# Kernel optimization log

Hardware: AMD Instinct MI355X
Metric: run time of the kernel (lower is better)

The kernel has to match this reference:

```python
import jax, jax.numpy as jnp
import numpy as np

L = 2
NB = (L + 1) ** 2      # 9 spherical-harmonic basis components
C = 256                # in_channels == out_channels
MID = C // 4           # 64, mid_channels in the FF
N = 4096               # nodes
K = 16                 # neighbors (neighbor_cg)


def _real_sh_l2(rel):
    # Real spherical harmonics up to l=2 of normalized edge directions. rel: [N,K,3] -> [N,K,9]
    r = jnp.sqrt(jnp.sum(rel * rel, axis=-1, keepdims=True))
    d = rel / (r + 1e-8)
    x, y, z = d[..., 0], d[..., 1], d[..., 2]
    c0 = 0.28209479177387814
    c1 = 0.4886025119029199
    c2 = 1.0925484305920792
    c2b = 0.31539156525252005
    c2c = 0.5462742152960396
    return jnp.stack([
        jnp.full_like(x, c0),
        c1 * y, c1 * z, c1 * x,
        c2 * x * y, c2 * y * z, c2b * (3.0 * z * z - 1.0), c2 * x * z, c2c * (x * x - y * y),
    ], axis=-1)


def setup_inputs() -> dict:
    key = jax.random.key(0)
    ks = jax.random.split(key, 8)
    return {
        "s_feats": jax.random.normal(ks[0], (N, NB, C), jnp.float32),
        "s_points": jax.random.normal(ks[1], (N, 3), jnp.float32),
        "cg": jax.random.normal(ks[2], (NB, NB, NB), jnp.float32) * 0.1,  # CG coefficient buffer
        "W_proj": jax.random.normal(ks[3], (C, C), jnp.float32) / np.sqrt(C),
        "ln_w": jnp.ones((L + 1, C), jnp.float32),
        "ln_b": jnp.zeros((C,), jnp.float32),
        "W_ff1": jax.random.normal(ks[4], (C, MID), jnp.float32) / np.sqrt(C),
        "W_gate": jax.random.normal(ks[5], (MID, MID * (L + 1)), jnp.float32) / np.sqrt(MID),
        "W_ff2": jax.random.normal(ks[6], (MID, C), jnp.float32) / np.sqrt(MID),
        "neighbor_indices": jax.random.randint(ks[7], (N, K), 0, N),
    }


def _forward(s_feats, s_points, cg, W_proj, ln_w, ln_b, W_ff1, W_gate, W_ff2, neighbor_indices):
    # --- CGConv: project, gather neighbors, SH of edge directions, CG tensor product, mean-aggregate ---
    h = jnp.einsum('nic,co->nio', s_feats, W_proj)               # [N,9,C]
    nbr = h[neighbor_indices]                                    # [N,K,9,C] irregular gather
    rel = s_points[neighbor_indices] - s_points[:, None, :]      # [N,K,3]
    sh = _real_sh_l2(rel)                                        # [N,K,9]
    x = jnp.einsum('nkic,nkj,ijo->noc', nbr, sh, cg) / K         # [N,9,C]
    # --- residual add of input (linear3 == Identity since in_channels == out_channels) ---
    x = x + s_feats
    shortcut = x
    # --- EquivariantLayerNormV2: per-degree RMS norm; mean-center + bias only on l=0 ---
    outs = []
    for l in range(L + 1):
        f = x[:, l * l:(l + 1) * (l + 1), :]                     # [N,2l+1,C]
        if l == 0:
            f = f - jnp.mean(f, axis=-1, keepdims=True)
        nrm = jnp.mean(f * f, axis=(1, 2), keepdims=True)
        f = f * jax.lax.rsqrt(nrm + 1e-5) * ln_w[l][None, None, :]
        if l == 0:
            f = f + ln_b[None, None, :]
        outs.append(f)
    y = jnp.concatenate(outs, axis=1)
    # --- FF: Linear -> Gate_3j -> Linear, residual ---
    z = jnp.einsum('nic,cm->nim', y, W_ff1)                      # [N,9,MID]
    after = z[:, 0, :] @ W_gate                                  # [N, MID*(L+1)]
    t0 = jax.nn.silu(after[:, :MID])
    mult = jax.nn.sigmoid(after[:, MID:])                        # [N, MID*L]
    gated = [t0[:, None, :]]
    for l in range(1, L + 1):
        gated.append(z[:, l * l:(l + 1) * (l + 1), :] * mult[:, None, (l - 1) * MID:l * MID])
    z = jnp.concatenate(gated, axis=1)                           # [N,9,MID]
    return jnp.einsum('nim,mc->nic', z, W_ff2) + shortcut


def reference(s_feats, s_points, cg, W_proj, ln_w, ln_b, W_ff1, W_gate, W_ff2, neighbor_indices):
    return _forward(s_feats, s_points, cg, W_proj, ln_w, ln_b, W_ff1, W_gate, W_ff2, neighbor_indices)
```

## Files before the change

kernel.cpp:

```cpp
#include <hip/hip_runtime.h>
#include <hip/hip_bf16.h>

#define N_PTS  4096
#define NB     9
#define C      256
#define MID    64
#define KNBR   16
#define NROWS  (N_PTS * NB)

typedef __attribute__((ext_vector_type(8))) short          short8;
typedef __attribute__((ext_vector_type(4))) float          f32x4;
typedef __attribute__((ext_vector_type(4))) unsigned short ush4;
typedef __attribute__((ext_vector_type(8))) unsigned short ush8;

static __device__ __forceinline__ unsigned short f2bf(float f) {
    union { __hip_bfloat16 h; unsigned short u; } cv;
    cv.h = __float2bfloat16(f);
    return cv.u;
}
static __device__ __forceinline__ float bf2f(unsigned short s) {
    union { unsigned u; float f; } v; v.u = ((unsigned)s) << 16;
    return v.f;
}
static __device__ __forceinline__ unsigned packbf(float a, float b) {
    return (unsigned)f2bf(a) | ((unsigned)f2bf(b) << 16);
}

__global__ __launch_bounds__(256) void k_prep(const float* __restrict__ Wp,
                                              const float* __restrict__ W1,
                                              const float* __restrict__ W2,
                                              unsigned short* __restrict__ Wpt,
                                              unsigned short* __restrict__ W1t,
                                              unsigned short* __restrict__ W2t) {
    __shared__ float T[32][33];
    const int b = blockIdx.x;
    const float* in; unsigned short* out; int K, N, kt, nt;
    if (b < 64)      { in = Wp; out = Wpt; K = 256; N = 256; kt = b >> 3;        nt = b & 7; }
    else if (b < 80) { in = W1; out = W1t; K = 256; N = 64;  kt = (b - 64) >> 1; nt = (b - 64) & 1; }
    else             { in = W2; out = W2t; K = 64;  N = 256; kt = (b - 80) >> 3; nt = (b - 80) & 7; }
    const int tx = threadIdx.x & 31;
    const int ty = threadIdx.x >> 5;
    const int k0 = kt * 32, n0 = nt * 32;
#pragma unroll
    for (int i = 0; i < 4; ++i)
        T[ty + i * 8][tx] = in[(size_t)(k0 + ty + i * 8) * N + n0 + tx];
    __syncthreads();
#pragma unroll
    for (int i = 0; i < 4; ++i)
        out[(size_t)(n0 + ty + i * 8) * K + k0 + tx] = f2bf(T[tx][ty + i * 8]);
}

#define LDK 40
__global__ __launch_bounds__(256) void k_proj(const float* __restrict__ A,
                                              const unsigned short* __restrict__ Wpt,
                                              unsigned short* __restrict__ H) {
    __shared__ unsigned short As[128 * LDK];
    __shared__ unsigned short Bs[128 * LDK];
    const int tid = threadIdx.x;
    const int r0  = blockIdx.x * 128;
    const int n0  = blockIdx.y * 128;
    const int wave = tid >> 6, lane = tid & 63;
    const int wm = wave >> 1, wn = wave & 1;
    const int lr = lane & 15, lg = lane >> 4;

    f32x4 acc[4][4];
#pragma unroll
    for (int a = 0; a < 4; ++a)
#pragma unroll
        for (int b = 0; b < 4; ++b) acc[a][b] = (f32x4){0.f, 0.f, 0.f, 0.f};

    for (int k0 = 0; k0 < C; k0 += 32) {
        __syncthreads();
#pragma unroll
        for (int rep = 0; rep < 4; ++rep) {
            const int e   = rep * 256 + tid;
            const int row = e >> 3;
            const int c4  = (e & 7) << 2;
            const float4 v = *reinterpret_cast<const float4*>(&A[(size_t)(r0 + row) * C + k0 + c4]);
            ush4 s = { f2bf(v.x), f2bf(v.y), f2bf(v.z), f2bf(v.w) };
            *reinterpret_cast<ush4*>(&As[row * LDK + c4]) = s;
        }
#pragma unroll
        for (int rep = 0; rep < 2; ++rep) {
            const int u   = rep * 256 + tid;
            const int row = u >> 2;
            const int seg = u & 3;
            *reinterpret_cast<ush8*>(&Bs[row * LDK + seg * 8]) =
                *reinterpret_cast<const ush8*>(&Wpt[(size_t)(n0 + row) * C + k0 + seg * 8]);
        }
        __syncthreads();

        short8 af[4], bfr[4];
#pragma unroll
        for (int mf = 0; mf < 4; ++mf)
            af[mf] = *reinterpret_cast<const short8*>(&As[(wm * 64 + mf * 16 + lr) * LDK + lg * 8]);
#pragma unroll
        for (int nf = 0; nf < 4; ++nf)
            bfr[nf] = *reinterpret_cast<const short8*>(&Bs[(wn * 64 + nf * 16 + lr) * LDK + lg * 8]);
#pragma unroll
        for (int mf = 0; mf < 4; ++mf)
#pragma unroll
            for (int nf = 0; nf < 4; ++nf)
                acc[mf][nf] = __builtin_amdgcn_mfma_f32_16x16x32_bf16(af[mf], bfr[nf], acc[mf][nf], 0, 0, 0);
    }
#pragma unroll
    for (int mf = 0; mf < 4; ++mf)
#pragma unroll
        for (int nf = 0; nf < 4; ++nf) {
            const int col = n0 + wn * 64 + nf * 16 + lr;
#pragma unroll
            for (int r = 0; r < 4; ++r) {
                const int row = r0 + wm * 64 + mf * 16 + lg * 4 + r;
                H[(size_t)row * C + col] = f2bf(acc[mf][nf][r]);
            }
        }
}

static __device__ __forceinline__ void load_chunk(const unsigned short* __restrict__ Hb,
                                                  const int* idx_s, int ki, int s,
                                                  ush8& q0, ush8& q1, ush8& q2, ush8& q3) {
    const int kk = ki / 9;
    const int ii = ki - kk * 9;
    const unsigned short* hrow = Hb + (size_t)(idx_s[kk] * NB + ii) * C + s * 32;
    q0 = *reinterpret_cast<const ush8*>(hrow + 0);
    q1 = *reinterpret_cast<const ush8*>(hrow + 8);
    q2 = *reinterpret_cast<const ush8*>(hrow + 16);
    q3 = *reinterpret_cast<const ush8*>(hrow + 24);
}
static __device__ __forceinline__ void stage_chunk(unsigned short* Bs, int r, int s, int nrows,
                                                   ush8 q0, ush8 q1, ush8 q2, ush8 q3) {
    if (r < nrows) {
        const unsigned short* qe;
        qe = reinterpret_cast<const unsigned short*>(&q0);
#pragma unroll
        for (int e = 0; e < 8; ++e) Bs[(s * 32 + e) * 40 + r] = qe[e];
        qe = reinterpret_cast<const unsigned short*>(&q1);
#pragma unroll
        for (int e = 0; e < 8; ++e) Bs[(s * 32 + 8 + e) * 40 + r] = qe[e];
        qe = reinterpret_cast<const unsigned short*>(&q2);
#pragma unroll
        for (int e = 0; e < 8; ++e) Bs[(s * 32 + 16 + e) * 40 + r] = qe[e];
        qe = reinterpret_cast<const unsigned short*>(&q3);
#pragma unroll
        for (int e = 0; e < 8; ++e) Bs[(s * 32 + 24 + e) * 40 + r] = qe[e];
    }
}

__global__ __launch_bounds__(256) void k_cg_ln(const unsigned short* __restrict__ Hb,
                                               const float* __restrict__ s_feats,
                                               const float* __restrict__ pts,
                                               const float* __restrict__ cg,
                                               const int*   __restrict__ nbr,
                                               unsigned short* __restrict__ Xb,
                                               float* __restrict__ scr) {
    __shared__ unsigned short Bs[256 * 40];
    __shared__ unsigned short wT[16 * 168];
    __shared__ float sh_s[KNBR][NB];
    __shared__ int   idx_s[KNBR];
    __shared__ float red_s[2][4];

    float* const cg_s = reinterpret_cast<float*>(Bs);

    const int tid  = threadIdx.x;
    const int n    = blockIdx.x;
    const int wv   = tid >> 6;
    const int lane = tid & 63;
    const int g16  = lane >> 4;
    const int l16  = lane & 15;

    {
        unsigned* w32 = reinterpret_cast<unsigned*>(wT);
        for (int e = tid; e < (16 * 168) / 2; e += 256) w32[e] = 0u;
    }
    for (int e = tid; e < 729; e += 256) cg_s[e] = cg[e];
    if (tid < KNBR) {
        const int idx = nbr[n * KNBR + tid];
        idx_s[tid] = idx;
        const float px = pts[idx * 3 + 0] - pts[n * 3 + 0];
        const float py = pts[idx * 3 + 1] - pts[n * 3 + 1];
        const float pz = pts[idx * 3 + 2] - pts[n * 3 + 2];
        const float r  = sqrtf(px * px + py * py + pz * pz);
        const float iv = 1.f / (r + 1e-8f);
        const float dx = px * iv, dy = py * iv, dz = pz * iv;
        const float c1 = 0.4886025119029199f;
        const float c2 = 1.0925484305920792f;
        sh_s[tid][0] = 0.28209479177387814f;
        sh_s[tid][1] = c1 * dy;
        sh_s[tid][2] = c1 * dz;
        sh_s[tid][3] = c1 * dx;
        sh_s[tid][4] = c2 * dx * dy;
        sh_s[tid][5] = c2 * dy * dz;
        sh_s[tid][6] = 0.31539156525252005f * (3.f * dz * dz - 1.f);
        sh_s[tid][7] = c2 * dx * dz;
        sh_s[tid][8] = 0.5462742152960396f * (dx * dx - dy * dy);
    }
    __syncthreads();

    const int r = tid & 31;
    const int s = tid >> 5;

    ush8 qa0, qa1, qa2, qa3, qb0, qb1, qb2, qb3;
    load_chunk(Hb, idx_s, 0 * 32 + r, s, qa0, qa1, qa2, qa3);
    load_chunk(Hb, idx_s, 1 * 32 + r, s, qb0, qb1, qb2, qb3);

    for (int t = tid; t < 144 * 9; t += 256) {
        const int ki = t / 9;
        const int o  = t - ki * 9;
        const int kk = ki / 9;
        const int ii = ki - kk * 9;
        float sv = 0.f;
#pragma unroll
        for (int j = 0; j < 9; ++j) sv = fmaf(sh_s[kk][j], cg_s[ii * 81 + j * 9 + o], sv);
        wT[o * 168 + ki] = f2bf(sv);
    }

    f32x4 acc[4];
#pragma unroll
    for (int i = 0; i < 4; ++i) acc[i] = (f32x4){0.f, 0.f, 0.f, 0.f};

#define MFMA_STEP(cc)                                                                   \
    do {                                                                                \
        const short8 af = *reinterpret_cast<const short8*>(&wT[l16 * 168 + (cc) * 32 + g16 * 8]); \
        short8 bfr[4];                                                                  \
        _Pragma("unroll")                                                               \
        for (int ti = 0; ti < 4; ++ti)                                                  \
            bfr[ti] = *reinterpret_cast<const short8*>(&Bs[(wv * 64 + ti * 16 + l16) * 40 + g16 * 8]); \
        _Pragma("unroll")                                                               \
        for (int ti = 0; ti < 4; ++ti)                                                  \
            acc[ti] = __builtin_amdgcn_mfma_f32_16x16x32_bf16(af, bfr[ti], acc[ti], 0, 0, 0); \
    } while (0)

    __syncthreads();
    stage_chunk(Bs, r, s, 32, qa0, qa1, qa2, qa3);
    load_chunk(Hb, idx_s, 2 * 32 + r, s, qa0, qa1, qa2, qa3);
    __syncthreads();
    MFMA_STEP(0);
    __syncthreads();
    stage_chunk(Bs, r, s, 32, qb0, qb1, qb2, qb3);
    load_chunk(Hb, idx_s, 3 * 32 + r, s, qb0, qb1, qb2, qb3);
    __syncthreads();
    MFMA_STEP(1);
    __syncthreads();
    stage_chunk(Bs, r, s, 32, qa0, qa1, qa2, qa3);
    if (r < 16) load_chunk(Hb, idx_s, 4 * 32 + r, s, qa0, qa1, qa2, qa3);
    __syncthreads();
    MFMA_STEP(2);
    __syncthreads();
    stage_chunk(Bs, r, s, 32, qb0, qb1, qb2, qb3);
    __syncthreads();
    MFMA_STEP(3);
    __syncthreads();
    stage_chunk(Bs, r, s, 16, qa0, qa1, qa2, qa3);
    __syncthreads();
    MFMA_STEP(4);
#undef MFMA_STEP

    __syncthreads();
    float* const Dld = reinterpret_cast<float*>(Bs);
#pragma unroll
    for (int ti = 0; ti < 4; ++ti) {
        const int cgl = (wv * 4 + ti) * 16 + l16;
#pragma unroll
        for (int rr = 0; rr < 4; ++rr) {
            const int o = g16 * 4 + rr;
            if (o < 9) Dld[o * 264 + cgl] = acc[ti][rr] * (1.f / (float)KNBR);
        }
    }
    __syncthreads();

    if (tid < 128) {
        const int c = tid * 2;
        const float* sf = s_feats + (size_t)n * (NB * C) + c;
        float2 xv[9];
#pragma unroll
        for (int i = 0; i < 9; ++i) {
            const float2 sv = *reinterpret_cast<const float2*>(&sf[(size_t)i * C]);
            xv[i].x = Dld[i * 264 + c]     + sv.x;
            xv[i].y = Dld[i * 264 + c + 1] + sv.y;
        }
        unsigned* xo = reinterpret_cast<unsigned*>(Xb + (size_t)n * (NB * C));
#pragma unroll
        for (int i = 0; i < 9; ++i) xo[i * 128 + tid] = packbf(xv[i].x, xv[i].y);

        float s0 = xv[0].x + xv[0].y;
        float s1 = xv[0].x * xv[0].x + xv[0].y * xv[0].y;
        float s2 = 0.f, s3 = 0.f;
#pragma unroll
        for (int o = 1; o < 4; ++o) s2 += xv[o].x * xv[o].x + xv[o].y * xv[o].y;
#pragma unroll
        for (int o = 4; o < 9; ++o) s3 += xv[o].x * xv[o].x + xv[o].y * xv[o].y;
#pragma unroll
        for (int off = 32; off >= 1; off >>= 1) {
            s0 += __shfl_xor(s0, off);
            s1 += __shfl_xor(s1, off);
            s2 += __shfl_xor(s2, off);
            s3 += __shfl_xor(s3, off);
        }
        if (lane == 0) {
            red_s[wv][0] = s0; red_s[wv][1] = s1;
            red_s[wv][2] = s2; red_s[wv][3] = s3;
        }
    }
    __syncthreads();
    if (tid == 0) {
        float* sp = scr + (size_t)n * 4;
        sp[0] = red_s[0][0] + red_s[1][0];
        sp[1] = red_s[0][1] + red_s[1][1];
        sp[2] = red_s[0][2] + red_s[1][2];
        sp[3] = red_s[0][3] + red_s[1][3];
    }
}

__global__ __launch_bounds__(256) void k_ff1(const unsigned short* __restrict__ Xb,
                                             const float* __restrict__ scr,
                                             const float* __restrict__ ln_w,
                                             const float* __restrict__ ln_b,
                                             const unsigned short* __restrict__ W1t,
                                             unsigned short* __restrict__ Zb) {
    __shared__ unsigned short As[128 * LDK];
    __shared__ unsigned short Bs[64 * LDK];
    const int tid = threadIdx.x;
    const int r0  = blockIdx.x * 128;
    const int wave = tid >> 6, lane = tid & 63;
    const int wm = wave >> 1, wn = wave & 1;
    const int lr = lane & 15, lg = lane >> 4;

    float mu_[4], rv_[4];
    int   cls_[4];
#pragma unroll
    for (int rep = 0; rep < 4; ++rep) {
        const int row = r0 + ((rep * 256 + tid) >> 3);
        const int nn  = row / 9;
        const int ii  = row - nn * 9;
        const float* sp = scr + (size_t)nn * 4;
        const float a0 = sp[0], a1 = sp[1], a2 = sp[2], a3 = sp[3];
        if (ii == 0) {
            const float mu = a0 * (1.f / 256.f);
            mu_[rep] = mu;
            rv_[rep] = rsqrtf(a1 * (1.f / 256.f) - mu * mu + 1e-5f);
            cls_[rep] = 0;
        } else if (ii < 4) {
            mu_[rep] = 0.f; rv_[rep] = rsqrtf(a2 * (1.f / 768.f) + 1e-5f); cls_[rep] = 1;
        } else {
            mu_[rep] = 0.f; rv_[rep] = rsqrtf(a3 * (1.f / 1280.f) + 1e-5f); cls_[rep] = 2;
        }
    }

    f32x4 acc[4][2];
#pragma unroll
    for (int a = 0; a < 4; ++a) { acc[a][0] = (f32x4){0.f,0.f,0.f,0.f}; acc[a][1] = (f32x4){0.f,0.f,0.f,0.f}; }

    for (int k0 = 0; k0 < C; k0 += 32) {
        __syncthreads();
#pragma unroll
        for (int rep = 0; rep < 4; ++rep) {
            const int e   = rep * 256 + tid;
            const int row = e >> 3;
            const int c4  = (e & 7) << 2;
            const ush4 xq = *reinterpret_cast<const ush4*>(&Xb[(size_t)(r0 + row) * C + k0 + c4]);
            const float4 lw = *reinterpret_cast<const float4*>(&ln_w[cls_[rep] * C + k0 + c4]);
            const float mu = mu_[rep], rv = rv_[rep];
            float yx = (bf2f(xq.x) - mu) * rv * lw.x;
            float yy = (bf2f(xq.y) - mu) * rv * lw.y;
            float yz = (bf2f(xq.z) - mu) * rv * lw.z;
            float yw = (bf2f(xq.w) - mu) * rv * lw.w;
            if (cls_[rep] == 0) {
                const float4 lb = *reinterpret_cast<const float4*>(&ln_b[k0 + c4]);
                yx += lb.x; yy += lb.y; yz += lb.z; yw += lb.w;
            }
            ush4 s = { f2bf(yx), f2bf(yy), f2bf(yz), f2bf(yw) };
            *reinterpret_cast<ush4*>(&As[row * LDK + c4]) = s;
        }
        {
            const int row = tid >> 2;
            const int seg = tid & 3;
            *reinterpret_cast<ush8*>(&Bs[row * LDK + seg * 8]) =
                *reinterpret_cast<const ush8*>(&W1t[(size_t)row * C + k0 + seg * 8]);
        }
        __syncthreads();

        short8 af[4], bfr[2];
#pragma unroll
        for (int mf = 0; mf < 4; ++mf)
            af[mf] = *reinterpret_cast<const short8*>(&As[(wm * 64 + mf * 16 + lr) * LDK + lg * 8]);
#pragma unroll
        for (int nf = 0; nf < 2; ++nf)
            bfr[nf] = *reinterpret_cast<const short8*>(&Bs[(wn * 32 + nf * 16 + lr) * LDK + lg * 8]);
#pragma unroll
        for (int mf = 0; mf < 4; ++mf)
#pragma unroll
            for (int nf = 0; nf < 2; ++nf)
                acc[mf][nf] = __builtin_amdgcn_mfma_f32_16x16x32_bf16(af[mf], bfr[nf], acc[mf][nf], 0, 0, 0);
    }
#pragma unroll
    for (int mf = 0; mf < 4; ++mf)
#pragma unroll
        for (int nf = 0; nf < 2; ++nf) {
            const int col = wn * 32 + nf * 16 + lr;
#pragma unroll
            for (int r = 0; r < 4; ++r) {
                const int row = r0 + wm * 64 + mf * 16 + lg * 4 + r;
                Zb[(size_t)row * MID + col] = f2bf(acc[mf][nf][r]);
            }
        }
}

__global__ __launch_bounds__(192) void k_gate(const unsigned short* __restrict__ Zb,
                                              const float* __restrict__ Wg,
                                              float* __restrict__ G) {
    __shared__ float wgs[64 * 192];
    __shared__ float z0s[16 * 64];
    const int tid = threadIdx.x;
    const int n0  = blockIdx.x * 16;

    for (int e = tid; e < 64 * 192; e += 192) wgs[e] = Wg[e];
    for (int e = tid; e < 16 * 64; e += 192) {
        const int r = e >> 6, m = e & 63;
        z0s[e] = bf2f(Zb[(size_t)(n0 + r) * (NB * MID) + m]);
    }
    __syncthreads();

    const int j = tid;
    for (int r = 0; r < 16; ++r) {
        float acc = 0.f;
        for (int m0 = 0; m0 < 64; m0 += 4) {
            const float4 zv = *reinterpret_cast<const float4*>(&z0s[r * 64 + m0]);
            acc = fmaf(zv.x, wgs[(m0 + 0) * 192 + j], acc);
            acc = fmaf(zv.y, wgs[(m0 + 1) * 192 + j], acc);
            acc = fmaf(zv.z, wgs[(m0 + 2) * 192 + j], acc);
            acc = fmaf(zv.w, wgs[(m0 + 3) * 192 + j], acc);
        }
        const float sig = 1.f / (1.f + expf(-acc));
        G[(size_t)(n0 + r) * 192 + j] = (j < 64) ? acc * sig : sig;
    }
}

#define LDK64 72
__global__ __launch_bounds__(256) void k_final(const unsigned short* __restrict__ Zb,
                                               const float* __restrict__ G,
                                               const unsigned short* __restrict__ W2t,
                                               const unsigned short* __restrict__ Xb,
                                               float* __restrict__ OUT) {
    __shared__ unsigned short As[128 * LDK64];
    __shared__ unsigned short Bs[128 * LDK64];
    const int tid = threadIdx.x;
    const int r0  = blockIdx.x * 128;
    const int n0  = blockIdx.y * 128;
    const int wave = tid >> 6, lane = tid & 63;
    const int wm = wave >> 1, wn = wave & 1;
    const int lr = lane & 15, lg = lane >> 4;

    {
        const int arow = tid >> 1;
        const int kh   = (tid & 1) * 32;
        const int grow = r0 + arow;
        const int nn   = grow / 9;
        const int ii   = grow - nn * 9;
        if (ii == 0) {
            const float* gp = &G[(size_t)nn * 192 + kh];
#pragma unroll
            for (int j = 0; j < 32; j += 4) {
                const float4 g = *reinterpret_cast<const float4*>(&gp[j]);
                ush4 s = { f2bf(g.x), f2bf(g.y), f2bf(g.z), f2bf(g.w) };
                *reinterpret_cast<ush4*>(&As[arow * LDK64 + kh + j]) = s;
            }
        } else {
            const float* gm = &G[(size_t)nn * 192 + ((ii < 4) ? 64 : 128) + kh];
            const unsigned short* zr = &Zb[(size_t)nn * (NB * MID) + ii * MID + kh];
#pragma unroll
            for (int j = 0; j < 32; j += 4) {
                const ush4 zv = *reinterpret_cast<const ush4*>(&zr[j]);
                const float4 g = *reinterpret_cast<const float4*>(&gm[j]);
                ush4 s = { f2bf(bf2f(zv.x) * g.x), f2bf(bf2f(zv.y) * g.y),
                           f2bf(bf2f(zv.z) * g.z), f2bf(bf2f(zv.w) * g.w) };
                *reinterpret_cast<ush4*>(&As[arow * LDK64 + kh + j]) = s;
            }
        }
    }
#pragma unroll
    for (int rep = 0; rep < 4; ++rep) {
        const int u   = rep * 256 + tid;
        const int row = u >> 3;
        const int seg = u & 7;
        *reinterpret_cast<ush8*>(&Bs[row * LDK64 + seg * 8]) =
            *reinterpret_cast<const ush8*>(&W2t[(size_t)(n0 + row) * MID + seg * 8]);
    }
    __syncthreads();

    f32x4 acc[4][4];
#pragma unroll
    for (int a = 0; a < 4; ++a)
#pragma unroll
        for (int b = 0; b < 4; ++b) acc[a][b] = (f32x4){0.f, 0.f, 0.f, 0.f};

#pragma unroll
    for (int ks = 0; ks < 2; ++ks) {
        short8 af[4], bfr[4];
#pragma unroll
        for (int mf = 0; mf < 4; ++mf)
            af[mf] = *reinterpret_cast<const short8*>(&As[(wm * 64 + mf * 16 + lr) * LDK64 + ks * 32 + lg * 8]);
#pragma unroll
        for (int nf = 0; nf < 4; ++nf)
            bfr[nf] = *reinterpret_cast<const short8*>(&Bs[(wn * 64 + nf * 16 + lr) * LDK64 + ks * 32 + lg * 8]);
#pragma unroll
        for (int mf = 0; mf < 4; ++mf)
#pragma unroll
            for (int nf = 0; nf < 4; ++nf)
                acc[mf][nf] = __builtin_amdgcn_mfma_f32_16x16x32_bf16(af[mf], bfr[nf], acc[mf][nf], 0, 0, 0);
    }

#pragma unroll
    for (int mf = 0; mf < 4; ++mf)
#pragma unroll
        for (int nf = 0; nf < 4; ++nf) {
            const int col = n0 + wn * 64 + nf * 16 + lr;
#pragma unroll
            for (int r = 0; r < 4; ++r) {
                const int row = r0 + wm * 64 + mf * 16 + lg * 4 + r;
                OUT[(size_t)row * C + col] = acc[mf][nf][r] + bf2f(Xb[(size_t)row * C + col]);
            }
        }
}

extern "C" void kernel_launch(void* const* d_in, const int* in_sizes, int n_in,
                              void* d_out, int out_size, void* d_ws, size_t ws_size,
                              hipStream_t stream) {
    const float* s_feats = (const float*)d_in[0];
    const float* s_pts   = (const float*)d_in[1];
    const float* cg      = (const float*)d_in[2];
    const float* W_proj  = (const float*)d_in[3];
    const float* ln_w    = (const float*)d_in[4];
    const float* ln_b    = (const float*)d_in[5];
    const float* W_ff1   = (const float*)d_in[6];
    const float* W_gate  = (const float*)d_in[7];
    const float* W_ff2   = (const float*)d_in[8];
    const int*   nbr     = (const int*)d_in[9];
    float* out = (float*)d_out;

    unsigned short* Hb  = (unsigned short*)d_ws;
    unsigned short* Xb  = Hb + (size_t)NROWS * C;
    unsigned short* Zb  = Xb + (size_t)NROWS * C;
    unsigned short* Wpt = Zb + (size_t)NROWS * MID;
    unsigned short* W1t = Wpt + 256 * 256;
    unsigned short* W2t = W1t + 64 * 256;
    float* G   = (float*)(W2t + 256 * 64);
    float* scr = G + (size_t)N_PTS * 192;

    k_prep  <<<96,                   256, 0, stream>>>(W_proj, W_ff1, W_ff2, Wpt, W1t, W2t);
    k_proj  <<<dim3(NROWS / 128, 2), 256, 0, stream>>>(s_feats, Wpt, Hb);
    k_cg_ln <<<N_PTS,                256, 0, stream>>>(Hb, s_feats, s_pts, cg, nbr, Xb, scr);
    k_ff1   <<<NROWS / 128,          256, 0, stream>>>(Xb, scr, ln_w, ln_b, W1t, Zb);
    k_gate  <<<N_PTS / 16,           192, 0, stream>>>(Zb, W_gate, G);
    k_final <<<dim3(NROWS / 128, 2), 256, 0, stream>>>(Zb, G, W2t, Xb, out);
}
```

Before: 117.7 us.

## Split CG gather kernel into two channel halves per node

The CG convolution kernel now launches two blocks per node, each handling 128 of the 256 channels, which halves the shared staging buffer and the accumulators per block. The per-node LayerNorm partial sums are written per half into a doubled scratch array, and the FF1 kernel adds the two halves together. This raises the number of blocks and lowers LDS and register use per block to improve occupancy and latency hiding on the irregular gather. The cost is that the SH and CG weight table, neighbor indices and setup work are recomputed in both blocks, and only 64 threads do the epilogue.

```diff
diff --git a/kernel.cpp b/kernel.cpp
--- a/kernel.cpp
+++ b/kernel.cpp
@@ -116,33 +116,24 @@
         }
 }
 
-static __device__ __forceinline__ void load_chunk(const unsigned short* __restrict__ Hb,
-                                                  const int* idx_s, int ki, int s,
-                                                  ush8& q0, ush8& q1, ush8& q2, ush8& q3) {
+static __device__ __forceinline__ void load_chunk2(const unsigned short* __restrict__ Hb,
+                                                   const int* idx_s, int ki, int c0, int s,
+                                                   ush8& q0, ush8& q1) {
     const int kk = ki / 9;
     const int ii = ki - kk * 9;
-    const unsigned short* hrow = Hb + (size_t)(idx_s[kk] * NB + ii) * C + s * 32;
+    const unsigned short* hrow = Hb + (size_t)(idx_s[kk] * NB + ii) * C + c0 + s * 16;
     q0 = *reinterpret_cast<const ush8*>(hrow + 0);
     q1 = *reinterpret_cast<const ush8*>(hrow + 8);
-    q2 = *reinterpret_cast<const ush8*>(hrow + 16);
-    q3 = *reinterpret_cast<const ush8*>(hrow + 24);
-}
-static __device__ __forceinline__ void stage_chunk(unsigned short* Bs, int r, int s, int nrows,
-                                                   ush8 q0, ush8 q1, ush8 q2, ush8 q3) {
+}
+static __device__ __forceinline__ void stage_chunk2(unsigned short* Bs, int r, int s, int nrows,
+                                                    ush8 q0, ush8 q1) {
     if (r < nrows) {
-        const unsigned short* qe;
-        qe = reinterpret_cast<const unsigned short*>(&q0);
-#pragma unroll
-        for (int e = 0; e < 8; ++e) Bs[(s * 32 + e) * 40 + r] = qe[e];
+        const unsigned short* qe = reinterpret_cast<const unsigned short*>(&q0);
+#pragma unroll
+        for (int e = 0; e < 8; ++e) Bs[(s * 16 + e) * 40 + r] = qe[e];
         qe = reinterpret_cast<const unsigned short*>(&q1);
 #pragma unroll
-        for (int e = 0; e < 8; ++e) Bs[(s * 32 + 8 + e) * 40 + r] = qe[e];
-        qe = reinterpret_cast<const unsigned short*>(&q2);
-#pragma unroll
-        for (int e = 0; e < 8; ++e) Bs[(s * 32 + 16 + e) * 40 + r] = qe[e];
-        qe = reinterpret_cast<const unsigned short*>(&q3);
-#pragma unroll
-        for (int e = 0; e < 8; ++e) Bs[(s * 32 + 24 + e) * 40 + r] = qe[e];
+        for (int e = 0; e < 8; ++e) Bs[(s * 16 + 8 + e) * 40 + r] = qe[e];
     }
 }
 
@@ -153,16 +144,18 @@
                                                const int*   __restrict__ nbr,
                                                unsigned short* __restrict__ Xb,
                                                float* __restrict__ scr) {
-    __shared__ unsigned short Bs[256 * 40];
+    __shared__ unsigned short Bs[128 * 40];
     __shared__ unsigned short wT[16 * 168];
     __shared__ float sh_s[KNBR][NB];
     __shared__ int   idx_s[KNBR];
-    __shared__ float red_s[2][4];
 
     float* const cg_s = reinterpret_cast<float*>(Bs);
 
     const int tid  = threadIdx.x;
-    const int n    = blockIdx.x;
+    const int bid  = blockIdx.x;
+    const int n    = bid >> 1;
+    const int half = bid & 1;
+    const int c0   = half * 128;
     const int wv   = tid >> 6;
     const int lane = tid & 63;
     const int g16  = lane >> 4;
@@ -199,9 +192,9 @@
     const int r = tid & 31;
     const int s = tid >> 5;
 
-    ush8 qa0, qa1, qa2, qa3, qb0, qb1, qb2, qb3;
-    load_chunk(Hb, idx_s, 0 * 32 + r, s, qa0, qa1, qa2, qa3);
-    load_chunk(Hb, idx_s, 1 * 32 + r, s, qb0, qb1, qb2, qb3);
+    ush8 qa0, qa1, qb0, qb1;
+    load_chunk2(Hb, idx_s, 0 * 32 + r, c0, s, qa0, qa1);
+    load_chunk2(Hb, idx_s, 1 * 32 + r, c0, s, qb0, qb1);
 
     for (int t = tid; t < 144 * 9; t += 256) {
         const int ki = t / 9;
@@ -214,43 +207,40 @@
         wT[o * 168 + ki] = f2bf(sv);
     }
 
-    f32x4 acc[4];
-#pragma unroll
-    for (int i = 0; i < 4; ++i) acc[i] = (f32x4){0.f, 0.f, 0.f, 0.f};
+    f32x4 acc[2];
+    acc[0] = (f32x4){0.f, 0.f, 0.f, 0.f};
+    acc[1] = (f32x4){0.f, 0.f, 0.f, 0.f};
 
 #define MFMA_STEP(cc)                                                                   \
     do {                                                                                \
         const short8 af = *reinterpret_cast<const short8*>(&wT[l16 * 168 + (cc) * 32 + g16 * 8]); \
-        short8 bfr[4];                                                                  \
-        _Pragma("unroll")                                                               \
-        for (int ti = 0; ti < 4; ++ti)                                                  \
-            bfr[ti] = *reinterpret_cast<const short8*>(&Bs[(wv * 64 + ti * 16 + l16) * 40 + g16 * 8]); \
-        _Pragma("unroll")                                                               \
-        for (int ti = 0; ti < 4; ++ti)                                                  \
-            acc[ti] = __builtin_amdgcn_mfma_f32_16x16x32_bf16(af, bfr[ti], acc[ti], 0, 0, 0); \
+        const short8 b0 = *reinterpret_cast<const short8*>(&Bs[(wv * 32 + l16) * 40 + g16 * 8]); \
+        const short8 b1 = *reinterpret_cast<const short8*>(&Bs[(wv * 32 + 16 + l16) * 40 + g16 * 8]); \
+        acc[0] = __builtin_amdgcn_mfma_f32_16x16x32_bf16(af, b0, acc[0], 0, 0, 0);      \
+        acc[1] = __builtin_amdgcn_mfma_f32_16x16x32_bf16(af, b1, acc[1], 0, 0, 0);      \
     } while (0)
 
     __syncthreads();
-    stage_chunk(Bs, r, s, 32, qa0, qa1, qa2, qa3);
-    load_chunk(Hb, idx_s, 2 * 32 + r, s, qa0, qa1, qa2, qa3);
+    stage_chunk2(Bs, r, s, 32, qa0, qa1);
+    load_chunk2(Hb, idx_s, 2 * 32 + r, c0, s, qa0, qa1);
     __syncthreads();
     MFMA_STEP(0);
     __syncthreads();
-    stage_chunk(Bs, r, s, 32, qb0, qb1, qb2, qb3);
-    load_chunk(Hb, idx_s, 3 * 32 + r, s, qb0, qb1, qb2, qb3);
+    stage_chunk2(Bs, r, s, 32, qb0, qb1);
+    load_chunk2(Hb, idx_s, 3 * 32 + r, c0, s, qb0, qb1);
     __syncthreads();
     MFMA_STEP(1);
     __syncthreads();
-    stage_chunk(Bs, r, s, 32, qa0, qa1, qa2, qa3);
-    if (r < 16) load_chunk(Hb, idx_s, 4 * 32 + r, s, qa0, qa1, qa2, qa3);
+    stage_chunk2(Bs, r, s, 32, qa0, qa1);
+    if (r < 16) load_chunk2(Hb, idx_s, 4 * 32 + r, c0, s, qa0, qa1);
     __syncthreads();
     MFMA_STEP(2);
     __syncthreads();
-    stage_chunk(Bs, r, s, 32, qb0, qb1, qb2, qb3);
+    stage_chunk2(Bs, r, s, 32, qb0, qb1);
     __syncthreads();
     MFMA_STEP(3);
     __syncthreads();
-    stage_chunk(Bs, r, s, 16, qa0, qa1, qa2, qa3);
+    stage_chunk2(Bs, r, s, 16, qa0, qa1);
     __syncthreads();
     MFMA_STEP(4);
 #undef MFMA_STEP
@@ -258,27 +248,27 @@
     __syncthreads();
     float* const Dld = reinterpret_cast<float*>(Bs);
 #pragma unroll
-    for (int ti = 0; ti < 4; ++ti) {
-        const int cgl = (wv * 4 + ti) * 16 + l16;
+    for (int tt = 0; tt < 2; ++tt) {
+        const int cl = wv * 32 + tt * 16 + l16;
 #pragma unroll
         for (int rr = 0; rr < 4; ++rr) {
             const int o = g16 * 4 + rr;
-            if (o < 9) Dld[o * 264 + cgl] = acc[ti][rr] * (1.f / (float)KNBR);
-        }
-    }
-    __syncthreads();
-
-    if (tid < 128) {
-        const int c = tid * 2;
-        const float* sf = s_feats + (size_t)n * (NB * C) + c;
+            if (o < 9) Dld[o * 132 + cl] = acc[tt][rr] * (1.f / (float)KNBR);
+        }
+    }
+    __syncthreads();
+
+    if (tid < 64) {
+        const int cl = tid * 2;
+        const float* sf = s_feats + (size_t)n * (NB * C) + c0 + cl;
         float2 xv[9];
 #pragma unroll
         for (int i = 0; i < 9; ++i) {
             const float2 sv = *reinterpret_cast<const float2*>(&sf[(size_t)i * C]);
-            xv[i].x = Dld[i * 264 + c]     + sv.x;
-            xv[i].y = Dld[i * 264 + c + 1] + sv.y;
-        }
-        unsigned* xo = reinterpret_cast<unsigned*>(Xb + (size_t)n * (NB * C));
+            xv[i].x = Dld[i * 132 + cl]     + sv.x;
+            xv[i].y = Dld[i * 132 + cl + 1] + sv.y;
+        }
+        unsigned* xo = reinterpret_cast<unsigned*>(Xb + (size_t)n * (NB * C) + c0);
 #pragma unroll
         for (int i = 0; i < 9; ++i) xo[i * 128 + tid] = packbf(xv[i].x, xv[i].y);
 
@@ -296,18 +286,10 @@
             s2 += __shfl_xor(s2, off);
             s3 += __shfl_xor(s3, off);
         }
-        if (lane == 0) {
-            red_s[wv][0] = s0; red_s[wv][1] = s1;
-            red_s[wv][2] = s2; red_s[wv][3] = s3;
-        }
-    }
-    __syncthreads();
-    if (tid == 0) {
-        float* sp = scr + (size_t)n * 4;
-        sp[0] = red_s[0][0] + red_s[1][0];
-        sp[1] = red_s[0][1] + red_s[1][1];
-        sp[2] = red_s[0][2] + red_s[1][2];
-        sp[3] = red_s[0][3] + red_s[1][3];
+        if (tid == 0) {
+            float* sp = scr + (size_t)n * 8 + half * 4;
+            sp[0] = s0; sp[1] = s1; sp[2] = s2; sp[3] = s3;
+        }
     }
 }
 
@@ -332,8 +314,9 @@
         const int row = r0 + ((rep * 256 + tid) >> 3);
         const int nn  = row / 9;
         const int ii  = row - nn * 9;
-        const float* sp = scr + (size_t)nn * 4;
-        const float a0 = sp[0], a1 = sp[1], a2 = sp[2], a3 = sp[3];
+        const float* sp = scr + (size_t)nn * 8;
+        const float a0 = sp[0] + sp[4], a1 = sp[1] + sp[5];
+        const float a2 = sp[2] + sp[6], a3 = sp[3] + sp[7];
         if (ii == 0) {
             const float mu = a0 * (1.f / 256.f);
             mu_[rep] = mu;
@@ -548,7 +531,7 @@
 
     k_prep  <<<96,                   256, 0, stream>>>(W_proj, W_ff1, W_ff2, Wpt, W1t, W2t);
     k_proj  <<<dim3(NROWS / 128, 2), 256, 0, stream>>>(s_feats, Wpt, Hb);
-    k_cg_ln <<<N_PTS,                256, 0, stream>>>(Hb, s_feats, s_pts, cg, nbr, Xb, scr);
+    k_cg_ln <<<N_PTS * 2,            256, 0, stream>>>(Hb, s_feats, s_pts, cg, nbr, Xb, scr);
     k_ff1   <<<NROWS / 128,          256, 0, stream>>>(Xb, scr, ln_w, ln_b, W1t, Zb);
     k_gate  <<<N_PTS / 16,           192, 0, stream>>>(Zb, W_gate, G);
     k_final <<<dim3(NROWS / 128, 2), 256, 0, stream>>>(Zb, G, W2t, Xb, out);
```

Result: no change. 119.7 us (+1.6%).
